# Performance work log

Hardware: AMD Instinct MI355X
Metric: run time of the kernel (lower is better)

Reference implementation:

```python
import jax, jax.numpy as jnp
import numpy as np

N_NODES = 50000
N_EDGES = 640000
N_SUPPORT = 3
D_IN = 128
D_OUT = 128


def setup_inputs() -> dict:
    key = jax.random.key(0)
    k = jax.random.split(key, 6)
    x = jax.random.normal(k[0], (N_NODES, D_IN), dtype=jnp.float32)
    edge_rows = jax.random.randint(k[1], (N_SUPPORT, N_EDGES), 0, N_NODES, dtype=jnp.int32)
    edge_cols = jax.random.randint(k[2], (N_SUPPORT, N_EDGES), 0, N_NODES, dtype=jnp.int32)
    edge_vals = jax.random.uniform(k[3], (N_SUPPORT, N_EDGES), dtype=jnp.float32)
    weights = jax.random.normal(k[4], (N_SUPPORT, D_IN, D_OUT), dtype=jnp.float32) * 0.05
    bias = jax.random.normal(k[5], (D_OUT,), dtype=jnp.float32) * 0.01
    return {"x": x, "edge_rows": edge_rows, "edge_cols": edge_cols,
            "edge_vals": edge_vals, "weights": weights, "bias": bias}


def reference(x, edge_rows, edge_cols, edge_vals, weights, bias):
    # Dense projection per support: [S, N, D_OUT]
    pre = jnp.einsum('nd,sdo->sno', x, weights)

    def spmm(rows, cols, vals, dense):
        # sparse [N,N] @ dense [N,D] via gather + scatter-add
        msgs = vals[:, None] * dense[cols]          # [E, D]
        return jax.ops.segment_sum(msgs, rows, num_segments=dense.shape[0])

    out = jax.vmap(spmm)(edge_rows, edge_cols, edge_vals, pre).sum(axis=0)
    return jax.nn.relu(out + bias)
```

## Files before the change

### kernel.cpp

```cpp
#include <hip/hip_runtime.h>

#define N_NODES 50000
#define N_EDGES 640000
#define N_SUP   3
#define D       128
#define NTOT    150000
#define E_TOT   1920000
#define NC      293
#define CAPC    7680
#define CAPB    9216
#define CTILE   2048
#define CTPS    313
#define SBLKS   (N_SUP * CTPS)
#define XCBLKS  6250
#define WBLKS   192
#define LDSTR   132

typedef __attribute__((ext_vector_type(2))) float f32x2;
typedef __attribute__((ext_vector_type(4))) float f32x4;
typedef __attribute__((ext_vector_type(8))) short s16x8;

__device__ __forceinline__ unsigned short f2bf(float f) {
    unsigned int u = __float_as_uint(f);
    u += 0x7FFFu + ((u >> 16) & 1u);
    return (unsigned short)(u >> 16);
}

__global__ __launch_bounds__(256) void prep_scatter(
    const int* __restrict__ rows, const int* __restrict__ cols,
    const float* __restrict__ vals, int* __restrict__ coarse_wptr,
    uint2* __restrict__ sortedA,
    const float4* __restrict__ x, ushort4* __restrict__ xb,
    const float* __restrict__ W, unsigned short* __restrict__ Wf)
{
    __shared__ int h[NC], base[NC];
    int tid = threadIdx.x;

    if (blockIdx.x >= SBLKS) {
        int gid = (blockIdx.x - SBLKS) * 256 + tid;
        if (gid < N_NODES * D / 4) {
            float4 v = x[gid];
            ushort4 o;
            o.x = f2bf(v.x); o.y = f2bf(v.y); o.z = f2bf(v.z); o.w = f2bf(v.w);
            xb[gid] = o;
        } else {
            int g2 = gid - N_NODES * D / 4;
            if (g2 < N_SUP * D * D) {
                int j    = g2 & 7;
                int lane = (g2 >> 3) & 63;
                int rest = g2 >> 9;
                int nt = rest & 7, kb = (rest >> 3) & 3, s = rest >> 5;
                int k = kb * 32 + ((lane >> 4) * 8) + j;
                int n = nt * 16 + (lane & 15);
                Wf[g2] = f2bf(W[((size_t)s * D + k) * D + n]);
            }
        }
        return;
    }

    for (int i = tid; i < NC; i += 256) h[i] = 0;
    __syncthreads();

    int s  = blockIdx.x / CTPS;
    int tb = (blockIdx.x % CTPS) * CTILE;
    int n  = N_EDGES - tb; if (n > CTILE) n = CTILE;
    const int*   rp = rows + (size_t)s * N_EDGES + tb;
    const int*   cp = cols + (size_t)s * N_EDGES + tb;
    const float* vp = vals + (size_t)s * N_EDGES + tb;

    int bk[8], grow[8];
    #pragma unroll
    for (int i = 0; i < 8; ++i) {
        int idx = tid + i * 256;
        bk[i] = -1;
        if (idx < n) {
            grow[i] = s * N_NODES + rp[idx];
            bk[i] = grow[i] >> 9;
            atomicAdd(&h[bk[i]], 1);
        }
    }
    __syncthreads();
    for (int i = tid; i < NC; i += 256) {
        base[i] = atomicAdd(&coarse_wptr[i], h[i]);
        h[i] = 0;
    }
    __syncthreads();
    #pragma unroll
    for (int i = 0; i < 8; ++i) {
        int idx = tid + i * 256;
        if (idx < n) {
            int rank = atomicAdd(&h[bk[i]], 1);
            int slot = base[bk[i]] + rank;
            if (slot < CAPC) {
                unsigned int meta = ((unsigned int)(grow[i] & 511) << 16)
                                  | (unsigned int)cp[idx];
                sortedA[(size_t)bk[i] * CAPC + slot] =
                    make_uint2(meta, __float_as_uint(vp[idx]));
            }
        }
    }
}

__global__ __launch_bounds__(512) void bucket_sort(
    const int* __restrict__ coarse_wptr, const uint2* __restrict__ sortedA,
    int* __restrict__ row_ptr2, unsigned int* __restrict__ sortedB)
{
    int c  = blockIdx.x >> 2;
    int q  = blockIdx.x & 3;
    int cnt = coarse_wptr[c];
    if (cnt > CAPC) cnt = CAPC;
    int rowlo = q * 128;

    __shared__ int hist[512];
    __shared__ int rank[128];
    __shared__ int fin[128];
    int tid = threadIdx.x;
    hist[tid] = 0;
    __syncthreads();

    const uint2* src = sortedA + (size_t)c * CAPC;
    for (int i = tid; i < cnt; i += 512)
        atomicAdd(&hist[src[i].x >> 16], 1);
    __syncthreads();

    int padded = (hist[tid] + 3) & ~3;
    hist[tid] = padded;
    __syncthreads();
    for (int off = 1; off < 512; off <<= 1) {
        int t = (tid >= off) ? hist[tid - off] : 0;
        __syncthreads();
        hist[tid] += t;
        __syncthreads();
    }
    int start = c * CAPB + hist[tid] - padded;
    if ((unsigned)(tid - rowlo) < 128u) {
        rank[tid - rowlo] = start;
        fin [tid - rowlo] = start + padded;
    }
    if (q == 0) {
        row_ptr2[c * 513 + tid] = start;
        if (tid == 511) row_ptr2[c * 513 + 512] = c * CAPB + hist[511];
    }
    __syncthreads();

    auto proc = [&](uint2 e) {
        int lr = (int)(e.x >> 16) - rowlo;
        if ((unsigned)lr < 128u) {
            int r = atomicAdd(&rank[lr], 1);
            sortedB[r] = ((unsigned int)f2bf(__uint_as_float(e.y)) << 16)
                       | (e.x & 0xFFFFu);
        }
    };
    int i = tid;
    for (; i + 1536 < cnt; i += 2048) {
        uint2 e0 = src[i], e1 = src[i + 512];
        uint2 e2 = src[i + 1024], e3 = src[i + 1536];
        proc(e0); proc(e1); proc(e2); proc(e3);
    }
    for (; i < cnt; i += 512) proc(src[i]);
    __syncthreads();

    if (tid < 128)
        for (int p = rank[tid]; p < fin[tid]; ++p) sortedB[p] = 0;
}

__global__ __launch_bounds__(256) void gather_gemm(
    const unsigned short* __restrict__ xb, const int* __restrict__ row_ptr2,
    const unsigned int* __restrict__ sortedB,
    const unsigned short* __restrict__ Wf,
    const float* __restrict__ bias, float* __restrict__ out)
{
    __shared__ unsigned short ys[48 * LDSTR];
    __shared__ int rs[48], re[48];
    const int tid  = threadIdx.x;
    const int w    = tid >> 6;
    const int lane = tid & 63;
    const int m0   = blockIdx.x * 16;

    if (tid < 48) {
        int grow = (tid >> 4) * N_NODES + m0 + (tid & 15);
        int rpi  = (grow >> 9) * 513 + (grow & 511);
        rs[tid] = row_ptr2[rpi];
        re[tid] = row_ptr2[rpi + 1];
    }
    __syncthreads();

    const int hh = lane >> 5;
    const int u  = lane & 31;
    for (int r = w; r < 48; r += 4) {
        int start = rs[r], end = re[r];
        f32x2 accA = {0.f, 0.f}, accB = {0.f, 0.f};
        for (int j = start; j < end; j += 64) {
            int m = end - j; if (m > 64) m = 64;
            unsigned int ev = (lane < m) ? sortedB[j + lane] : 0u;
            for (int t = 0; t < m; t += 4) {
                unsigned int e0 = (unsigned int)__shfl((int)ev, t + hh);
                unsigned int e1 = (unsigned int)__shfl((int)ev, t + 2 + hh);
                float v0 = __uint_as_float(e0 & 0xFFFF0000u);
                float v1 = __uint_as_float(e1 & 0xFFFF0000u);
                uint2 X0 = *((const uint2*)(xb + (size_t)(e0 & 0xFFFFu) * D) + u);
                uint2 X1 = *((const uint2*)(xb + (size_t)(e1 & 0xFFFFu) * D) + u);
                f32x2 xa0 = {__uint_as_float(X0.x << 16),
                             __uint_as_float(X0.x & 0xFFFF0000u)};
                f32x2 xb0 = {__uint_as_float(X0.y << 16),
                             __uint_as_float(X0.y & 0xFFFF0000u)};
                f32x2 xa1 = {__uint_as_float(X1.x << 16),
                             __uint_as_float(X1.x & 0xFFFF0000u)};
                f32x2 xb1 = {__uint_as_float(X1.y << 16),
                             __uint_as_float(X1.y & 0xFFFF0000u)};
                accA += v0 * xa0;
                accB += v0 * xb0;
                accA += v1 * xa1;
                accB += v1 * xb1;
            }
        }
        float a0 = accA.x, a1 = accA.y, a2 = accB.x, a3 = accB.y;
        a0 += __shfl_xor(a0, 32);
        a1 += __shfl_xor(a1, 32);
        a2 += __shfl_xor(a2, 32);
        a3 += __shfl_xor(a3, 32);
        if (hh == 0) {
            uint2 o;
            o.x = (unsigned int)f2bf(a0) | ((unsigned int)f2bf(a1) << 16);
            o.y = (unsigned int)f2bf(a2) | ((unsigned int)f2bf(a3) << 16);
            *(uint2*)(ys + r * LDSTR + u * 4) = o;
        }
    }
    __syncthreads();

    const int quad = lane >> 4;
    const int l16  = lane & 15;
    const int nt0  = w * 2;
    f32x4 acc0 = {0.f, 0.f, 0.f, 0.f}, acc1 = {0.f, 0.f, 0.f, 0.f};

    #pragma unroll
    for (int s = 0; s < N_SUP; ++s) {
        #pragma unroll
        for (int kb = 0; kb < 4; ++kb) {
            union { uint2 q[2]; s16x8 v; } A;
            const unsigned short* ap = ys + (s * 16 + l16) * LDSTR
                                          + kb * 32 + quad * 8;
            A.q[0] = *(const uint2*)ap;
            A.q[1] = *(const uint2*)(ap + 4);
            const unsigned short* wf = Wf + (size_t)((s * 4 + kb) * 8 + nt0) * 64 * 8
                                          + lane * 8;
            s16x8 b0 = *(const s16x8*)wf;
            s16x8 b1 = *(const s16x8*)(wf + 64 * 8);
            acc0 = __builtin_amdgcn_mfma_f32_16x16x32_bf16(A.v, b0, acc0, 0, 0, 0);
            acc1 = __builtin_amdgcn_mfma_f32_16x16x32_bf16(A.v, b1, acc1, 0, 0, 0);
        }
    }

    #pragma unroll
    for (int p = 0; p < 2; ++p) {
        int col = (nt0 + p) * 16 + l16;
        float bv = bias[col];
        f32x4 a = p ? acc1 : acc0;
        #pragma unroll
        for (int r = 0; r < 4; ++r) {
            int row = m0 + quad * 4 + r;
            out[(size_t)row * D + col] = fmaxf(a[r] + bv, 0.f);
        }
    }
}

extern "C" void kernel_launch(void* const* d_in, const int* in_sizes, int n_in,
                              void* d_out, int out_size, void* d_ws, size_t ws_size,
                              hipStream_t stream)
{
    const float* x         = (const float*)d_in[0];
    const int*   edge_rows = (const int*)  d_in[1];
    const int*   edge_cols = (const int*)  d_in[2];
    const float* edge_vals = (const float*)d_in[3];
    const float* weights   = (const float*)d_in[4];
    const float* bias      = (const float*)d_in[5];
    float* out = (float*)d_out;

    char* ws = (char*)d_ws;
    size_t off = 0;
    auto alloc = [&](size_t bytes) -> char* {
        char* p = ws + off;
        off += (bytes + 255) & ~(size_t)255;
        return p;
    };
    int*            coarse_wptr = (int*)            alloc(NC * 4);
    int*            row_ptr2    = (int*)            alloc((size_t)NC * 513 * 4);
    unsigned short* xb          = (unsigned short*) alloc((size_t)N_NODES * D * 2);
    unsigned short* Wf          = (unsigned short*) alloc((size_t)N_SUP * D * D * 2);
    uint2*          sortedA     = (uint2*)          alloc((size_t)NC * CAPC * 8);
    unsigned int*   sortedB     = (unsigned int*)   alloc((size_t)NC * CAPB * 4);

    hipMemsetAsync(coarse_wptr, 0, NC * 4, stream);
    prep_scatter<<<SBLKS + XCBLKS + WBLKS, 256, 0, stream>>>(
        edge_rows, edge_cols, edge_vals, coarse_wptr, sortedA,
        (const float4*)x, (ushort4*)xb, weights, Wf);
    bucket_sort <<<NC * 4, 512, 0, stream>>>(coarse_wptr, sortedA,
                                             row_ptr2, sortedB);
    gather_gemm <<<N_NODES / 16, 256, 0, stream>>>(xb, row_ptr2, sortedB,
                                                   Wf, bias, out);
}
```

Measured before the change: 228.4 us.

## Stage coarse-bucket scatter in LDS and use one sort block per bucket

prep_scatter now runs 512-thread blocks. Each block builds a per-tile prefix sum over coarse buckets and stages its edges in LDS, sorted by bucket, so the global writes to sortedA are grouped into contiguous runs instead of scattered. bucket_sort moves from four blocks per coarse bucket, each rereading the whole bucket, to one block that loads its edges into registers once and handles all 512 rows. This cuts redundant global reads and improves write coalescing, at the cost of more LDS per block, a large register array and fewer blocks for the sort stage.

```diff
diff --git a/kernel.cpp b/kernel.cpp
--- a/kernel.cpp
+++ b/kernel.cpp
@@ -12,8 +12,8 @@
 #define CTILE   2048
 #define CTPS    313
 #define SBLKS   (N_SUP * CTPS)
-#define XCBLKS  6250
-#define WBLKS   192
+#define XCBLKS  3125
+#define WBLKS   96
 #define LDSTR   132
 
 typedef __attribute__((ext_vector_type(2))) float f32x2;
@@ -26,18 +26,17 @@
     return (unsigned short)(u >> 16);
 }
 
-__global__ __launch_bounds__(256) void prep_scatter(
+__global__ __launch_bounds__(512) void prep_scatter(
     const int* __restrict__ rows, const int* __restrict__ cols,
     const float* __restrict__ vals, int* __restrict__ coarse_wptr,
     uint2* __restrict__ sortedA,
     const float4* __restrict__ x, ushort4* __restrict__ xb,
     const float* __restrict__ W, unsigned short* __restrict__ Wf)
 {
-    __shared__ int h[NC], base[NC];
     int tid = threadIdx.x;
 
     if (blockIdx.x >= SBLKS) {
-        int gid = (blockIdx.x - SBLKS) * 256 + tid;
+        int gid = (blockIdx.x - SBLKS) * 512 + tid;
         if (gid < N_NODES * D / 4) {
             float4 v = x[gid];
             ushort4 o;
@@ -58,7 +57,13 @@
         return;
     }
 
-    for (int i = tid; i < NC; i += 256) h[i] = 0;
+    __shared__ int          h[512];
+    __shared__ int          toff[512];
+    __shared__ int          gbase[512];
+    __shared__ uint2        stage[CTILE];
+    __shared__ unsigned int dst[CTILE];
+
+    h[tid] = 0;
     __syncthreads();
 
     int s  = blockIdx.x / CTPS;
@@ -68,36 +73,48 @@
     const int*   cp = cols + (size_t)s * N_EDGES + tb;
     const float* vp = vals + (size_t)s * N_EDGES + tb;
 
-    int bk[8], grow[8];
-    #pragma unroll
-    for (int i = 0; i < 8; ++i) {
-        int idx = tid + i * 256;
+    int bk[4], rk[4]; uint2 ed[4];
+    #pragma unroll
+    for (int i = 0; i < 4; ++i) {
+        int idx = tid + i * 512;
         bk[i] = -1;
         if (idx < n) {
-            grow[i] = s * N_NODES + rp[idx];
-            bk[i] = grow[i] >> 9;
-            atomicAdd(&h[bk[i]], 1);
-        }
-    }
-    __syncthreads();
-    for (int i = tid; i < NC; i += 256) {
-        base[i] = atomicAdd(&coarse_wptr[i], h[i]);
-        h[i] = 0;
-    }
-    __syncthreads();
-    #pragma unroll
-    for (int i = 0; i < 8; ++i) {
-        int idx = tid + i * 256;
-        if (idx < n) {
-            int rank = atomicAdd(&h[bk[i]], 1);
-            int slot = base[bk[i]] + rank;
-            if (slot < CAPC) {
-                unsigned int meta = ((unsigned int)(grow[i] & 511) << 16)
-                                  | (unsigned int)cp[idx];
-                sortedA[(size_t)bk[i] * CAPC + slot] =
-                    make_uint2(meta, __float_as_uint(vp[idx]));
-            }
-        }
+            int grow = s * N_NODES + rp[idx];
+            bk[i] = grow >> 9;
+            rk[i] = atomicAdd(&h[bk[i]], 1);
+            ed[i] = make_uint2(((unsigned int)(grow & 511) << 16)
+                               | (unsigned int)cp[idx],
+                               __float_as_uint(vp[idx]));
+        }
+    }
+    __syncthreads();
+    int cntb = h[tid];
+    __syncthreads();
+    for (int off = 1; off < 512; off <<= 1) {
+        int t = (tid >= off) ? h[tid - off] : 0;
+        __syncthreads();
+        h[tid] += t;
+        __syncthreads();
+    }
+    toff[tid]  = h[tid] - cntb;
+    gbase[tid] = (cntb > 0) ? atomicAdd(&coarse_wptr[tid], cntb) : 0;
+    __syncthreads();
+
+    #pragma unroll
+    for (int i = 0; i < 4; ++i) {
+        if (bk[i] >= 0) {
+            int slot = toff[bk[i]] + rk[i];
+            int gslot = gbase[bk[i]] + rk[i];
+            stage[slot] = ed[i];
+            dst[slot] = (gslot < CAPC)
+                      ? (unsigned int)(bk[i] * CAPC + gslot)
+                      : 0xFFFFFFFFu;
+        }
+    }
+    __syncthreads();
+    for (int j = tid; j < n; j += 512) {
+        unsigned int d = dst[j];
+        if (d != 0xFFFFFFFFu) sortedA[d] = stage[j];
     }
 }
 
@@ -105,22 +122,29 @@
     const int* __restrict__ coarse_wptr, const uint2* __restrict__ sortedA,
     int* __restrict__ row_ptr2, unsigned int* __restrict__ sortedB)
 {
-    int c  = blockIdx.x >> 2;
-    int q  = blockIdx.x & 3;
+    int c  = blockIdx.x;
     int cnt = coarse_wptr[c];
     if (cnt > CAPC) cnt = CAPC;
-    int rowlo = q * 128;
 
     __shared__ int hist[512];
-    __shared__ int rank[128];
-    __shared__ int fin[128];
+    __shared__ int rank[512];
+    __shared__ int fin[512];
     int tid = threadIdx.x;
     hist[tid] = 0;
-    __syncthreads();
 
     const uint2* src = sortedA + (size_t)c * CAPC;
-    for (int i = tid; i < cnt; i += 512)
-        atomicAdd(&hist[src[i].x >> 16], 1);
+    uint2 e[15];
+    #pragma unroll
+    for (int k = 0; k < 15; ++k) {
+        int idx = tid + k * 512;
+        if (idx < cnt) e[k] = src[idx];
+    }
+    __syncthreads();
+    #pragma unroll
+    for (int k = 0; k < 15; ++k) {
+        int idx = tid + k * 512;
+        if (idx < cnt) atomicAdd(&hist[e[k].x >> 16], 1);
+    }
     __syncthreads();
 
     int padded = (hist[tid] + 3) & ~3;
@@ -133,35 +157,23 @@
         __syncthreads();
     }
     int start = c * CAPB + hist[tid] - padded;
-    if ((unsigned)(tid - rowlo) < 128u) {
-        rank[tid - rowlo] = start;
-        fin [tid - rowlo] = start + padded;
-    }
-    if (q == 0) {
-        row_ptr2[c * 513 + tid] = start;
-        if (tid == 511) row_ptr2[c * 513 + 512] = c * CAPB + hist[511];
-    }
-    __syncthreads();
-
-    auto proc = [&](uint2 e) {
-        int lr = (int)(e.x >> 16) - rowlo;
-        if ((unsigned)lr < 128u) {
-            int r = atomicAdd(&rank[lr], 1);
-            sortedB[r] = ((unsigned int)f2bf(__uint_as_float(e.y)) << 16)
-                       | (e.x & 0xFFFFu);
-        }
-    };
-    int i = tid;
-    for (; i + 1536 < cnt; i += 2048) {
-        uint2 e0 = src[i], e1 = src[i + 512];
-        uint2 e2 = src[i + 1024], e3 = src[i + 1536];
-        proc(e0); proc(e1); proc(e2); proc(e3);
-    }
-    for (; i < cnt; i += 512) proc(src[i]);
-    __syncthreads();
-
-    if (tid < 128)
-        for (int p = rank[tid]; p < fin[tid]; ++p) sortedB[p] = 0;
+    rank[tid] = start;
+    fin [tid] = start + padded;
+    row_ptr2[c * 513 + tid] = start;
+    if (tid == 511) row_ptr2[c * 513 + 512] = c * CAPB + hist[511];
+    __syncthreads();
+
+    #pragma unroll
+    for (int k = 0; k < 15; ++k) {
+        int idx = tid + k * 512;
+        if (idx < cnt) {
+            int r = atomicAdd(&rank[e[k].x >> 16], 1);
+            sortedB[r] = ((unsigned int)f2bf(__uint_as_float(e[k].y)) << 16)
+                       | (e[k].x & 0xFFFFu);
+        }
+    }
+    __syncthreads();
+    for (int p = rank[tid]; p < fin[tid]; ++p) sortedB[p] = 0;
 }
 
 __global__ __launch_bounds__(256) void gather_gemm(
@@ -283,19 +295,19 @@
         off += (bytes + 255) & ~(size_t)255;
         return p;
     };
-    int*            coarse_wptr = (int*)            alloc(NC * 4);
+    int*            coarse_wptr = (int*)            alloc(512 * 4);
     int*            row_ptr2    = (int*)            alloc((size_t)NC * 513 * 4);
     unsigned short* xb          = (unsigned short*) alloc((size_t)N_NODES * D * 2);
     unsigned short* Wf          = (unsigned short*) alloc((size_t)N_SUP * D * D * 2);
     uint2*          sortedA     = (uint2*)          alloc((size_t)NC * CAPC * 8);
     unsigned int*   sortedB     = (unsigned int*)   alloc((size_t)NC * CAPB * 4);
 
-    hipMemsetAsync(coarse_wptr, 0, NC * 4, stream);
-    prep_scatter<<<SBLKS + XCBLKS + WBLKS, 256, 0, stream>>>(
+    hipMemsetAsync(coarse_wptr, 0, 512 * 4, stream);
+    prep_scatter<<<SBLKS + XCBLKS + WBLKS, 512, 0, stream>>>(
         edge_rows, edge_cols, edge_vals, coarse_wptr, sortedA,
         (const float4*)x, (ushort4*)xb, weights, Wf);
-    bucket_sort <<<NC * 4, 512, 0, stream>>>(coarse_wptr, sortedA,
-                                             row_ptr2, sortedB);
+    bucket_sort <<<NC, 512, 0, stream>>>(coarse_wptr, sortedA,
+                                         row_ptr2, sortedB);
     gather_gemm <<<N_NODES / 16, 256, 0, stream>>>(xb, row_ptr2, sortedB,
                                                    Wf, bias, out);
 }
```

New measurement: 198.2 us. 13.2% less time.
